# Kernel optimization log

Hardware: AMD Instinct MI355X
Metric: run time of the kernel (lower is better)

The kernel has to match this reference:

```python
import jax, jax.numpy as jnp
import numpy as np

C = 512
H_HEADS = 8
CTX_D = 768
GEO_D = 512
FFN_D = 4 * C
EPS = 1e-5


def _layernorm(x, g, b):
    mu = jnp.mean(x, axis=-1, keepdims=True)
    var = jnp.mean((x - mu) ** 2, axis=-1, keepdims=True)
    return (x - mu) * jax.lax.rsqrt(var + EPS) * g + b


def _cross_attn(x, ctx, Wq, Wk, Wv, Wo, bo, h):
    # x: (B, N, C), ctx: (B, S, Dctx)
    b, n, _ = x.shape
    s = ctx.shape[1]
    inner = Wq.shape[1]
    d = inner // h
    q = (x @ Wq).reshape(b, n, h, d)
    k = (ctx @ Wk).reshape(b, s, h, d)
    v = (ctx @ Wv).reshape(b, s, h, d)
    sim = jnp.einsum('bihd,bjhd->bhij', q, k) * (d ** -0.5)
    attn = jax.nn.softmax(sim, axis=-1)
    out = jnp.einsum('bhij,bjhd->bihd', attn, v).reshape(b, n, inner)
    return out @ Wo + bo


def setup_inputs() -> dict:
    key = jax.random.key(0)
    ks = jax.random.split(key, 24)
    std = lambda fan_in: 1.0 / np.sqrt(fan_in)
    inp = {
        'x': jax.random.normal(ks[0], (4, C, 64, 64), jnp.float32),
        'context': jax.random.normal(ks[1], (4, 77, CTX_D), jnp.float32),
        'geometry_tokens': jax.random.normal(ks[2], (4, 256, GEO_D), jnp.float32),
        # layernorm params (norm1..norm4)
        'g1': jnp.ones((C,)), 'b1': jnp.zeros((C,)),
        'g2': jnp.ones((C,)), 'b2': jnp.zeros((C,)),
        'g3': jnp.ones((C,)), 'b3': jnp.zeros((C,)),
        'g4': jnp.ones((C,)), 'b4': jnp.zeros((C,)),
        # cross-attention (context) weights
        'cWq': jax.random.normal(ks[3], (C, C)) * std(C),
        'cWk': jax.random.normal(ks[4], (CTX_D, C)) * std(CTX_D),
        'cWv': jax.random.normal(ks[5], (CTX_D, C)) * std(CTX_D),
        'cWo': jax.random.normal(ks[6], (C, C)) * std(C),
        'cbo': jnp.zeros((C,)),
        # geometry-attention weights
        'gWq': jax.random.normal(ks[7], (C, C)) * std(C),
        'gWk': jax.random.normal(ks[8], (GEO_D, C)) * std(GEO_D),
        'gWv': jax.random.normal(ks[9], (GEO_D, C)) * std(GEO_D),
        'gWo': jax.random.normal(ks[10], (C, C)) * std(C),
        'gbo': jnp.zeros((C,)),
        # FFN weights
        'W1': jax.random.normal(ks[11], (C, FFN_D)) * std(C),
        'bf1': jnp.zeros((FFN_D,)),
        'W2': jax.random.normal(ks[12], (FFN_D, C)) * std(FFN_D),
        'bf2': jnp.zeros((C,)),
    }
    return inp


def reference(x, context, geometry_tokens,
              g1, b1, g2, b2, g3, b3, g4, b4,
              cWq, cWk, cWv, cWo, cbo,
              gWq, gWk, gWv, gWo, gbo,
              W1, bf1, W2, bf2):
    b, c, h, w = x.shape
    t = x.reshape(b, c, h * w).transpose(0, 2, 1)  # (B, N, C)
    # self_attn is called with context=None -> identity, so this is t + norm1(t)
    t = t + _layernorm(t, g1, b1)
    t = t + _cross_attn(_layernorm(t, g2, b2), context, cWq, cWk, cWv, cWo, cbo, H_HEADS)
    t = t + _cross_attn(_layernorm(t, g3, b3), geometry_tokens, gWq, gWk, gWv, gWo, gbo, H_HEADS)
    hdn = jax.nn.gelu(_layernorm(t, g4, b4) @ W1 + bf1, approximate=False)
    t = t + hdn @ W2 + bf2
    return t.transpose(0, 2, 1).reshape(b, c, h, w)
```

## Files before the change

### kernel.cpp

```cpp
#include <hip/hip_runtime.h>
#include <hip/hip_bf16.h>

using bf16 = __hip_bfloat16;
typedef __attribute__((ext_vector_type(8))) short short8;
typedef __attribute__((ext_vector_type(4))) short short4v;
typedef __attribute__((ext_vector_type(4))) float floatx4;

#define DEVFN __device__ __forceinline__

DEVFN float bf2f(bf16 v) { return __bfloat162float(v); }
DEVFN bf16 f2bf(float v) { return __float2bfloat16(v); }
DEVFN float us2f(unsigned short u) {
    union { unsigned int i; float f; } c; c.i = ((unsigned int)u) << 16; return c.f;
}
DEVFN unsigned short f2bfbits(float v) {
    union { bf16 h; unsigned short u; } c; c.h = f2bf(v); return c.u;
}
DEVFN float loadF(const void* p, size_t i, int isf) {
    return isf ? ((const float*)p)[i] : us2f(((const unsigned short*)p)[i]);
}
DEVFN void gl_lds16(const bf16* g, short* l) {
    __builtin_amdgcn_global_load_lds(
        (const __attribute__((address_space(1))) unsigned int*)g,
        (__attribute__((address_space(3))) unsigned int*)l, 16, 0, 0);
}
DEVFN float fast_gelu(float v) {
    float u = v * (0.7978845608028654f + 0.0356774081f * v * v);
    float e = __expf(2.f * u);
    float th = 1.f - 2.f / (e + 1.f);
    return 0.5f * v * (1.f + th);
}

__global__ __launch_bounds__(256) void detect_kernel(const void* x, int* flag)
{
    __shared__ int any;
    if (threadIdx.x == 0) any = 0;
    __syncthreads();
    const unsigned short* p = (const unsigned short*)x;
    int hit = 0;
    for (int i = threadIdx.x; i < 8192; i += 256) {
        if ((p[i] & 0x7F80u) == 0x7F80u) hit = 1;
    }
    if (hit) any = 1;
    __syncthreads();
    if (threadIdx.x == 0) flag[0] = any;
}

struct CVTab {
    const void* src[14];
    bf16* dst[14];
    int cnt[14];
    int bstart[14];
};
__global__ __launch_bounds__(256) void convert_batch_kernel(
    CVTab tab, const int* __restrict__ flag)
{
    int isf = *flag;
    int b = blockIdx.x;
    int s = 0;
#pragma unroll
    for (int i = 1; i < 14; i++) if (b >= tab.bstart[i]) s = i;
    const void* src = tab.src[s];
    bf16* dst = tab.dst[s];
    int cnt = tab.cnt[s];
    int base = (b - tab.bstart[s]) * 2048;
    int lim = min(base + 2048, cnt);
    for (int i = base + (int)threadIdx.x; i < lim; i += 256)
        dst[i] = f2bf(loadF(src, i, isf));
}

__global__ __launch_bounds__(256) void ln_in_kernel(
    const void* __restrict__ x, float* __restrict__ t,
    const bf16* __restrict__ g1c, const bf16* __restrict__ b1c,
    const bf16* __restrict__ g2c, const bf16* __restrict__ b2c,
    bf16* __restrict__ u,
    const int* __restrict__ flag, int NN)
{
    __shared__ float tile[16][516];
    int isf = *flag;
    int b = blockIdx.y;
    int n0 = blockIdx.x * 16;
    int tid = threadIdx.x;
    int nx = tid & 15, cy = tid >> 4;
#pragma unroll
    for (int p = 0; p < 32; p++) {
        int c = p * 16 + cy;
        tile[nx][c] = loadF(x, ((size_t)b * 512 + c) * NN + n0 + nx, isf);
    }
    __syncthreads();
    int w = tid >> 6, lane = tid & 63;
    for (int rr = 0; rr < 4; rr++) {
        int r = w * 4 + rr;
        float4 v0 = *(const float4*)&tile[r][lane * 8];
        float4 v1 = *(const float4*)&tile[r][lane * 8 + 4];
        float vals[8] = {v0.x, v0.y, v0.z, v0.w, v1.x, v1.y, v1.z, v1.w};
        float s = 0.f;
#pragma unroll
        for (int i = 0; i < 8; i++) s += vals[i];
#pragma unroll
        for (int off = 32; off; off >>= 1) s += __shfl_xor(s, off, 64);
        float mu = s * (1.f / 512.f);
        float sq = 0.f;
#pragma unroll
        for (int i = 0; i < 8; i++) { float d = vals[i] - mu; sq += d * d; }
#pragma unroll
        for (int off = 32; off; off >>= 1) sq += __shfl_xor(sq, off, 64);
        float rs = rsqrtf(sq * (1.f / 512.f) + 1e-5f);
        float out[8];
#pragma unroll
        for (int i = 0; i < 8; i++) {
            int c = lane * 8 + i;
            out[i] = vals[i] + (vals[i] - mu) * rs * bf2f(g1c[c]) + bf2f(b1c[c]);
        }
        size_t rbase = ((size_t)b * NN + n0 + r) * 512 + lane * 8;
        float* tp = t + rbase;
        *(float4*)tp = make_float4(out[0], out[1], out[2], out[3]);
        *(float4*)(tp + 4) = make_float4(out[4], out[5], out[6], out[7]);
        float s2 = 0.f;
#pragma unroll
        for (int i = 0; i < 8; i++) s2 += out[i];
#pragma unroll
        for (int off = 32; off; off >>= 1) s2 += __shfl_xor(s2, off, 64);
        float mu2 = s2 * (1.f / 512.f);
        float sq2 = 0.f;
#pragma unroll
        for (int i = 0; i < 8; i++) { float d = out[i] - mu2; sq2 += d * d; }
#pragma unroll
        for (int off = 32; off; off >>= 1) sq2 += __shfl_xor(sq2, off, 64);
        float rs2 = rsqrtf(sq2 * (1.f / 512.f) + 1e-5f);
        short4v uo[2];
#pragma unroll
        for (int i = 0; i < 8; i++) {
            int c = lane * 8 + i;
            uo[i >> 2][i & 3] =
                (short)f2bfbits((out[i] - mu2) * rs2 * bf2f(g2c[c]) + bf2f(b2c[c]));
        }
        *(short4v*)((unsigned short*)u + rbase) = uo[0];
        *(short4v*)((unsigned short*)u + rbase + 4) = uo[1];
    }
}

__global__ __launch_bounds__(256) void ln_res_kernel(
    const float* __restrict__ t, const bf16* __restrict__ r1,
    const bf16* __restrict__ r2,
    const bf16* __restrict__ g, const bf16* __restrict__ bta,
    bf16* __restrict__ outp, int Mrows)
{
    int w = threadIdx.x >> 6, lane = threadIdx.x & 63;
    int row = blockIdx.x * 4 + w;
    if (row >= Mrows) return;
    size_t base = (size_t)row * 512 + lane * 8;
    float4 v0 = *(const float4*)(t + base);
    float4 v1 = *(const float4*)(t + base + 4);
    float vals[8] = {v0.x, v0.y, v0.z, v0.w, v1.x, v1.y, v1.z, v1.w};
    {
        short8 a = *(const short8*)((const unsigned short*)r1 + base);
#pragma unroll
        for (int i = 0; i < 8; i++) vals[i] += us2f(((unsigned short*)&a)[i]);
    }
    if (r2) {
        short8 a = *(const short8*)((const unsigned short*)r2 + base);
#pragma unroll
        for (int i = 0; i < 8; i++) vals[i] += us2f(((unsigned short*)&a)[i]);
    }
    float s = 0.f;
#pragma unroll
    for (int i = 0; i < 8; i++) s += vals[i];
#pragma unroll
    for (int off = 32; off; off >>= 1) s += __shfl_xor(s, off, 64);
    float mu = s * (1.f / 512.f);
    float sq = 0.f;
#pragma unroll
    for (int i = 0; i < 8; i++) { float d = vals[i] - mu; sq += d * d; }
#pragma unroll
    for (int off = 32; off; off >>= 1) sq += __shfl_xor(sq, off, 64);
    float rs = rsqrtf(sq * (1.f / 512.f) + 1e-5f);
    short4v uo[2];
#pragma unroll
    for (int i = 0; i < 8; i++) {
        int c = lane * 8 + i;
        uo[i >> 2][i & 3] =
            (short)f2bfbits((vals[i] - mu) * rs * bf2f(g[c]) + bf2f(bta[c]));
    }
    *(short4v*)((unsigned short*)outp + base) = uo[0];
    *(short4v*)((unsigned short*)outp + base + 4) = uo[1];
}

__global__ __launch_bounds__(256) void transpose_out_kernel(
    const float* __restrict__ t, const bf16* __restrict__ rc,
    const bf16* __restrict__ rg, const bf16* __restrict__ f,
    void* __restrict__ o, const int* __restrict__ flag,
    int C, int NN)
{
    __shared__ float tile[32][33];
    int isf = *flag;
    int b = blockIdx.z;
    int n0 = blockIdx.x * 32, c0 = blockIdx.y * 32;
    int tx = threadIdx.x, ty = threadIdx.y;
#pragma unroll
    for (int i = 0; i < 4; i++) {
        size_t idx = ((size_t)b * NN + n0 + ty + i * 8) * C + c0 + tx;
        tile[ty + i * 8][tx] = t[idx] + bf2f(rc[idx]) + bf2f(rg[idx]) + bf2f(f[idx]);
    }
    __syncthreads();
#pragma unroll
    for (int i = 0; i < 4; i++) {
        size_t oi = ((size_t)b * C + c0 + ty + i * 8) * NN + n0 + tx;
        float val = tile[tx][ty + i * 8];
        if (isf) ((float*)o)[oi] = val;
        else ((bf16*)o)[oi] = f2bf(val);
    }
}

struct TWTab {
    const void* src[10];
    bf16* dst[10];
    int K[10];
    int Nc[10];
    int tstart[10];
};
__global__ __launch_bounds__(256) void transpose_w_batch(
    TWTab tab, const int* __restrict__ flag)
{
    __shared__ float tile[32][33];
    int isf = *flag;
    int b = blockIdx.x;
    int s = 0;
#pragma unroll
    for (int i = 1; i < 10; i++) if (b >= tab.tstart[i]) s = i;
    const void* Wm = tab.src[s];
    bf16* WT = tab.dst[s];
    int K = tab.K[s], Nc = tab.Nc[s];
    int lt = b - tab.tstart[s];
    int ntx = Nc >> 5;
    int n0 = (lt % ntx) * 32, k0 = (lt / ntx) * 32;
    int tx = threadIdx.x, ty = threadIdx.y;
#pragma unroll
    for (int i = 0; i < 4; i++)
        tile[ty + i * 8][tx] = loadF(Wm, (size_t)(k0 + ty + i * 8) * Nc + n0 + tx, isf);
    __syncthreads();
#pragma unroll
    for (int i = 0; i < 4; i++)
        WT[(size_t)(n0 + ty + i * 8) * K + k0 + tx] = f2bf(tile[tx][ty + i * 8]);
}

template <int MODE>
__global__ __launch_bounds__(256) void gemm64x2(
    const bf16* __restrict__ A,
    const bf16* __restrict__ WT0, const bf16* __restrict__ WT1,
    bf16* __restrict__ o0, bf16* __restrict__ o1,
    int M, int K, int Nc)
{
    const bf16* WT = blockIdx.z ? WT1 : WT0;
    bf16* outp = blockIdx.z ? o1 : o0;
    __shared__ short As[64 * 32];
    __shared__ short Bs[64 * 32];
    const int tid = threadIdx.x;
    const int m0 = blockIdx.y * 64;
    const int n0 = blockIdx.x * 64;
    const int w = tid >> 6;
    const int lane = tid & 63;
    const int lm = lane & 15;
    const int lq = lane >> 4;

    floatx4 acc[4];
#pragma unroll
    for (int nb = 0; nb < 4; nb++) acc[nb] = (floatx4){0.f, 0.f, 0.f, 0.f};

    const int srow = tid >> 2;
    const int scol = (tid & 3) << 3;
    const int agrow = m0 + srow;
    const bool aok = agrow < M;
    const bf16* Aptr = A + (size_t)agrow * K + scol;
    const bf16* Bptr = WT + (size_t)(n0 + srow) * K + scol;

    for (int k0 = 0; k0 < K; k0 += 32) {
        __syncthreads();
        int4 av = make_int4(0, 0, 0, 0);
        if (aok) av = *(const int4*)(Aptr + k0);
        *(int4*)(&As[srow * 32 + scol]) = av;
        *(int4*)(&Bs[srow * 32 + scol]) = *(const int4*)(Bptr + k0);
        __syncthreads();
        short8 a = *(const short8*)(&As[(w * 16 + lm) * 32 + lq * 8]);
#pragma unroll
        for (int nb = 0; nb < 4; nb++) {
            short8 b = *(const short8*)(&Bs[(nb * 16 + lm) * 32 + lq * 8]);
            acc[nb] = __builtin_amdgcn_mfma_f32_16x16x32_bf16(a, b, acc[nb], 0, 0, 0);
        }
    }

#pragma unroll
    for (int nb = 0; nb < 4; nb++) {
        int col = n0 + nb * 16 + lm;
#pragma unroll
        for (int r = 0; r < 4; r++) {
            int row = m0 + w * 16 + lq * 4 + r;
            if (row < M) {
                float v = acc[nb][r];
                if (MODE == 1) v = fast_gelu(v);
                outp[(size_t)row * Nc + col] = f2bf(v);
            }
        }
    }
}

#define MFMA_PAIR(RB, A00, A01, A10, A11)                                              \
    _Pragma("unroll")                                                                   \
    for (int cb = 0; cb < CB; cb++) {                                                   \
        acc[cb][RB]     = __builtin_amdgcn_mfma_f32_16x16x32_bf16(bf0[cb], A00, acc[cb][RB], 0, 0, 0);     \
        acc[cb][RB]     = __builtin_amdgcn_mfma_f32_16x16x32_bf16(bf1[cb], A01, acc[cb][RB], 0, 0, 0);     \
        acc[cb][RB + 1] = __builtin_amdgcn_mfma_f32_16x16x32_bf16(bf0[cb], A10, acc[cb][RB + 1], 0, 0, 0); \
        acc[cb][RB + 1] = __builtin_amdgcn_mfma_f32_16x16x32_bf16(bf1[cb], A11, acc[cb][RB + 1], 0, 0, 0); \
    }

template <int MODE, int CB>
__global__ __launch_bounds__(512, 2) void gemm8p(
    const bf16* __restrict__ A, const bf16* __restrict__ WT,
    const bf16* __restrict__ bias, void* __restrict__ outp,
    int K, int Nc)
{
    constexpr int BN = CB * 64;
    constexpr int ABUF = 256 * 64;
    constexpr int BBUF = BN * 64;
    __shared__ short As[2 * ABUF];
    __shared__ short Bs[2 * BBUF];

    const int tid = threadIdx.x;
    const int gx = gridDim.x;
    int g = blockIdx.y * gx + blockIdx.x;
    const int cpx = (gx * gridDim.y) >> 3;
    g = (g & 7) * cpx + (g >> 3);
    const int m0 = (g / gx) * 256;
    const int n0 = (g % gx) * BN;

    const int w = tid >> 6, lane = tid & 63;
    const int lm = lane & 15, lq = lane >> 4;
    const int wm = w >> 2, wn = w & 3;

    floatx4 acc[CB][8];
#pragma unroll
    for (int cb = 0; cb < CB; cb++)
#pragma unroll
        for (int rb = 0; rb < 8; rb++) acc[cb][rb] = (floatx4){0.f, 0.f, 0.f, 0.f};

    const int rbaseA = (tid >> 3) + ((tid >= 256) ? 96 : 0);
    const int chk = (((tid & 7) ^ ((tid >> 3) & 7)) << 3);
    const bf16* pA = A + (size_t)(m0 + rbaseA) * K + chk;
    const int rbaseB = ((tid >> 7) << (CB == 4 ? 6 : 5)) + ((tid >> 3) & 15);
    const bf16* pB = WT + (size_t)(n0 + rbaseB) * K + chk;
    const int wbA = w * 512 + ((w >= 4) ? 6144 : 0);
    const int wbB = (CB == 4) ? ((w >> 1) * 4096 + (w & 1) * 512)
                              : ((w >> 1) * 2048 + (w & 1) * 512);
    const size_t K32 = (size_t)K * 32;
    const size_t K16 = (size_t)K * 16;

    const int arow = (wm * 128 + lm) * 64;
    const int brow = (wn * CB * 16 + lm) * 64;
    const int sl0 = ((lq ^ (lm & 7)) << 3);
    const int sl1 = (((4 + lq) ^ (lm & 7)) << 3);

    const int nt = K >> 6;

#pragma unroll
    for (int q = 0; q < 4; q++) gl_lds16(pA + (size_t)q * K32, As + q * 2048 + wbA);
    if constexpr (CB == 4) {
        gl_lds16(pB,           Bs + wbB);
        gl_lds16(pB + K16,     Bs + 1024 + wbB);
        gl_lds16(pB + 2 * K16, Bs + 2048 + wbB);
        gl_lds16(pB + 3 * K16, Bs + 3072 + wbB);
    } else {
        gl_lds16(pB,       Bs + wbB);
        gl_lds16(pB + K16, Bs + 1024 + wbB);
    }
    {
        const bf16* qA = pA + 64;
        const bf16* qB = pB + 64;
        if constexpr (CB == 4) {
            gl_lds16(qB,           Bs + BBUF + wbB);
            gl_lds16(qB + K16,     Bs + BBUF + 1024 + wbB);
            gl_lds16(qB + 2 * K16, Bs + BBUF + 2048 + wbB);
            gl_lds16(qB + 3 * K16, Bs + BBUF + 3072 + wbB);
            gl_lds16(qA,           As + ABUF + wbA);
            gl_lds16(qA + K32,     As + ABUF + 2048 + wbA);
            asm volatile("s_waitcnt vmcnt(6)\n\ts_barrier" ::: "memory");
        } else {
            gl_lds16(qB,           Bs + BBUF + wbB);
            gl_lds16(qB + K16, Bs + BBUF + 1024 + wbB);
            gl_lds16(qA,           As + ABUF + wbA);
            gl_lds16(qA + K32,     As + ABUF + 2048 + wbA);
            gl_lds16(qA + 2 * K32, As + ABUF + 4096 + wbA);
            asm volatile("s_waitcnt vmcnt(5)\n\ts_barrier" ::: "memory");
        }
    }

    for (int s = 0; s < nt; ++s) {
        const int cu = s & 1;
        const short* cA = As + cu * ABUF;
        const short* cB = Bs + cu * BBUF;
        short* oA = As + (cu ^ 1) * ABUF;
        short* sA = As + cu * ABUF;
        short* sB = Bs + cu * BBUF;
        const bf16* pA1 = pA + (s + 1) * 64;
        const bf16* pA2 = pA + (s + 2) * 64;
        const bf16* pB2 = pB + (s + 2) * 64;
        short8 bf0[CB], bf1[CB], x0, x1, y0, y1;

#pragma unroll
        for (int cb = 0; cb < CB; cb++) {
            bf0[cb] = *(const short8*)&cB[brow + cb * 1024 + sl0];
            bf1[cb] = *(const short8*)&cB[brow + cb * 1024 + sl1];
        }
        x0 = *(const short8*)&cA[arow + sl0];
        x1 = *(const short8*)&cA[arow + sl1];
        y0 = *(const short8*)&cA[arow + 1024 + sl0];
        y1 = *(const short8*)&cA[arow + 1024 + sl1];
        if (s + 1 < nt) {
            if constexpr (CB == 4) {
                gl_lds16(pA1 + 2 * K32, oA + 2 * 2048 + wbA);
                gl_lds16(pA1 + 3 * K32, oA + 3 * 2048 + wbA);
            } else {
                gl_lds16(pA1 + 3 * K32, oA + 3 * 2048 + wbA);
            }
        }
        __builtin_amdgcn_s_setprio(1);
        MFMA_PAIR(0, x0, x1, y0, y1)
        __builtin_amdgcn_s_setprio(0);
        asm volatile("s_waitcnt lgkmcnt(0)\n\ts_barrier" ::: "memory");

        x0 = *(const short8*)&cA[arow + 2 * 1024 + sl0];
        x1 = *(const short8*)&cA[arow + 2 * 1024 + sl1];
        y0 = *(const short8*)&cA[arow + 3 * 1024 + sl0];
        y1 = *(const short8*)&cA[arow + 3 * 1024 + sl1];
        if (s + 2 < nt) {
            gl_lds16(pB2,       sB + wbB);
            gl_lds16(pB2 + K16, sB + 1024 + wbB);
        }
        __builtin_amdgcn_s_setprio(1);
        MFMA_PAIR(2, x0, x1, y0, y1)
        __builtin_amdgcn_s_setprio(0);
        asm volatile("s_waitcnt lgkmcnt(0)\n\ts_barrier" ::: "memory");

        x0 = *(const short8*)&cA[arow + 4 * 1024 + sl0];
        x1 = *(const short8*)&cA[arow + 4 * 1024 + sl1];
        y0 = *(const short8*)&cA[arow + 5 * 1024 + sl0];
        y1 = *(const short8*)&cA[arow + 5 * 1024 + sl1];
        if (s + 2 < nt) {
            if constexpr (CB == 4) {
                gl_lds16(pB2 + 2 * K16, sB + 2048 + wbB);
                gl_lds16(pB2 + 3 * K16, sB + 3072 + wbB);
            } else {
                gl_lds16(pA2, sA + wbA);
            }
        }
        __builtin_amdgcn_s_setprio(1);
        MFMA_PAIR(4, x0, x1, y0, y1)
        __builtin_amdgcn_s_setprio(0);
        asm volatile("s_waitcnt lgkmcnt(0)\n\ts_barrier" ::: "memory");

        x0 = *(const short8*)&cA[arow + 6 * 1024 + sl0];
        x1 = *(const short8*)&cA[arow + 6 * 1024 + sl1];
        y0 = *(const short8*)&cA[arow + 7 * 1024 + sl0];
        y1 = *(const short8*)&cA[arow + 7 * 1024 + sl1];
        if (s + 2 < nt) {
            if constexpr (CB == 4) {
                gl_lds16(pA2,       sA + wbA);
                gl_lds16(pA2 + K32, sA + 2048 + wbA);
            } else {
                gl_lds16(pA2 + K32,     sA + 2048 + wbA);
                gl_lds16(pA2 + 2 * K32, sA + 4096 + wbA);
            }
        }
        __builtin_amdgcn_s_setprio(1);
        MFMA_PAIR(6, x0, x1, y0, y1)
        __builtin_amdgcn_s_setprio(0);
        if (s <= nt - 3) {
            if constexpr (CB == 4)
                asm volatile("s_waitcnt vmcnt(6) lgkmcnt(0)\n\ts_barrier" ::: "memory");
            else
                asm volatile("s_waitcnt vmcnt(5) lgkmcnt(0)\n\ts_barrier" ::: "memory");
        } else if (s == nt - 2) {
            asm volatile("s_waitcnt vmcnt(0) lgkmcnt(0)\n\ts_barrier" ::: "memory");
        } else {
            asm volatile("s_waitcnt lgkmcnt(0)\n\ts_barrier" ::: "memory");
        }
    }
    __syncthreads();

    float4 bias4[CB];
#pragma unroll
    for (int cb = 0; cb < CB; cb++) {
        if (bias) {
            const bf16* bp = bias + n0 + wn * (CB * 16) + cb * 16 + lq * 4;
            bias4[cb] = make_float4(bf2f(bp[0]), bf2f(bp[1]), bf2f(bp[2]), bf2f(bp[3]));
        } else {
            bias4[cb] = make_float4(0.f, 0.f, 0.f, 0.f);
        }
    }

    if constexpr (MODE == 2) {
        float* po = (float*)outp;
#pragma unroll
        for (int rb = 0; rb < 8; rb++) {
            size_t m = m0 + wm * 128 + rb * 16 + lm;
#pragma unroll
            for (int cb = 0; cb < CB; cb++) {
                float* p = po + m * Nc + n0 + wn * (CB * 16) + cb * 16 + lq * 4;
                float4 f = *(float4*)p;
                f.x += acc[cb][rb][0] + bias4[cb].x;
                f.y += acc[cb][rb][1] + bias4[cb].y;
                f.z += acc[cb][rb][2] + bias4[cb].z;
                f.w += acc[cb][rb][3] + bias4[cb].w;
                *(float4*)p = f;
            }
        }
    } else if constexpr (CB == 2) {
        unsigned short* op = (unsigned short*)outp;
#pragma unroll
        for (int rb = 0; rb < 8; rb++) {
            size_t m = m0 + wm * 128 + rb * 16 + lm;
#pragma unroll
            for (int cb = 0; cb < 2; cb++) {
                short4v pk;
#pragma unroll
                for (int r = 0; r < 4; r++) {
                    float vv = acc[cb][rb][r] + ((const float*)&bias4[cb])[r];
                    if (MODE == 1) vv = fast_gelu(vv);
                    pk[r] = (short)f2bfbits(vv);
                }
                *(short4v*)(op + m * Nc + n0 + wn * 32 + cb * 16 + lq * 4) = pk;
            }
        }
    } else {
        unsigned short* stgb = (unsigned short*)&As[w * 1024];
        unsigned short* op = (unsigned short*)outp;
#pragma unroll
        for (int rb = 0; rb < 8; rb++) {
#pragma unroll
            for (int cb = 0; cb < 4; cb++) {
                short4v pk;
#pragma unroll
                for (int r = 0; r < 4; r++) {
                    float vv = acc[cb][rb][r] + ((const float*)&bias4[cb])[r];
                    if (MODE == 1) vv = fast_gelu(vv);
                    pk[r] = (short)f2bfbits(vv);
                }
                int chunk = (cb * 2 + (lq >> 1)) ^ (lm & 7);
                *(short4v*)(&stgb[lm * 64 + chunk * 8 + (lq & 1) * 4]) = pk;
            }
#pragma unroll
            for (int p = 0; p < 2; p++) {
                int row = p * 8 + (lane >> 3);
                int chunk = lane & 7;
                short8 ov = *(const short8*)(&stgb[row * 64 + ((chunk ^ (row & 7)) * 8)]);
                size_t m = m0 + wm * 128 + rb * 16 + row;
                *(short8*)(op + m * Nc + n0 + wn * 64 + chunk * 8) = ov;
            }
        }
    }
}

template <int SPAD, int SVALID>
__global__ __launch_bounds__(256) void attn_mfma_kernel(
    const bf16* __restrict__ q, const bf16* __restrict__ k, const bf16* __restrict__ v,
    bf16* __restrict__ o, int N)
{
    constexpr int MB = SPAD / 16;
    constexpr int KS = SPAD / 32;
    __shared__ unsigned short lds[SPAD * 64 + 64 * SPAD];
    unsigned short* Ks = lds;
    unsigned short* Vt = lds + SPAD * 64;
    unsigned short* Pw = lds;

    const int tid = threadIdx.x;
    const int b = blockIdx.x >> 3;
    const int h = blockIdx.x & 7;
    const int n0 = blockIdx.y * 64;
    const int w = tid >> 6, lane = tid & 63;
    const int lm = lane & 15, lq = lane >> 4;

    const unsigned short* kp = (const unsigned short*)k;
    const unsigned short* vp = (const unsigned short*)v;
    for (int idx = tid * 8; idx < SPAD * 64; idx += 2048) {
        int s = idx >> 6, d0 = idx & 63;
        short8 kv = {0, 0, 0, 0, 0, 0, 0, 0};
        short8 vv = {0, 0, 0, 0, 0, 0, 0, 0};
        if (s < SVALID) {
            size_t gb = ((size_t)(b * SVALID + s)) * 512 + h * 64 + d0;
            kv = *(const short8*)(kp + gb);
            vv = *(const short8*)(vp + gb);
        }
        int kc = (d0 >> 3) ^ (s & 7);
        *(short8*)(&Ks[s * 64 + kc * 8]) = kv;
        const unsigned short* vvp = (const unsigned short*)&vv;
#pragma unroll
        for (int i = 0; i < 8; i++) {
            int d = d0 + i;
            int sc = (s >> 3) ^ (d & 7);
            Vt[d * SPAD + sc * 8 + (s & 7)] = vvp[i];
        }
    }

    const int q0 = n0 + w * 16;
    const unsigned short* qp = (const unsigned short*)q;
    size_t qbase = ((size_t)(b * N + q0 + lm)) * 512 + h * 64 + lq * 8;
    short8 qf0 = *(const short8*)(qp + qbase);
    short8 qf1 = *(const short8*)(qp + qbase + 32);
    __syncthreads();

    floatx4 sacc[MB];
#pragma unroll
    for (int mb = 0; mb < MB; mb++) sacc[mb] = (floatx4){0.f, 0.f, 0.f, 0.f};
#pragma unroll
    for (int mb = 0; mb < MB; mb++) {
        int srow = mb * 16 + lm;
        short8 a0 = *(const short8*)(&Ks[srow * 64 + ((lq ^ (lm & 7)) * 8)]);
        short8 a1 = *(const short8*)(&Ks[srow * 64 + (((4 + lq) ^ (lm & 7)) * 8)]);
        sacc[mb] = __builtin_amdgcn_mfma_f32_16x16x32_bf16(a0, qf0, sacc[mb], 0, 0, 0);
        sacc[mb] = __builtin_amdgcn_mfma_f32_16x16x32_bf16(a1, qf1, sacc[mb], 0, 0, 0);
    }

    float mx = -1e30f;
#pragma unroll
    for (int mb = 0; mb < MB; mb++)
#pragma unroll
        for (int r = 0; r < 4; r++) {
            int s = mb * 16 + lq * 4 + r;
            if (s < SVALID) mx = fmaxf(mx, sacc[mb][r]);
        }
    mx = fmaxf(mx, __shfl_xor(mx, 16, 64));
    mx = fmaxf(mx, __shfl_xor(mx, 32, 64));
    mx *= 0.125f;
    float sum = 0.f;
#pragma unroll
    for (int mb = 0; mb < MB; mb++)
#pragma unroll
        for (int r = 0; r < 4; r++) {
            int s = mb * 16 + lq * 4 + r;
            float e = (s < SVALID) ? __expf(sacc[mb][r] * 0.125f - mx) : 0.f;
            sacc[mb][r] = e;
            sum += e;
        }
    sum += __shfl_xor(sum, 16, 64);
    sum += __shfl_xor(sum, 32, 64);
    float inv = 1.f / sum;

    __syncthreads();

    unsigned short* Pme = Pw + w * 16 * SPAD;
#pragma unroll
    for (int mb = 0; mb < MB; mb++) {
        short4v pk;
        pk[0] = (short)f2bfbits(sacc[mb][0] * inv);
        pk[1] = (short)f2bfbits(sacc[mb][1] * inv);
        pk[2] = (short)f2bfbits(sacc[mb][2] * inv);
        pk[3] = (short)f2bfbits(sacc[mb][3] * inv);
        int chunk = (mb * 2 + (lq >> 1)) ^ (lm & 7);
        *(short4v*)(&Pme[lm * SPAD + chunk * 8 + (lq & 1) * 4]) = pk;
    }

    floatx4 oacc[4];
#pragma unroll
    for (int mb2 = 0; mb2 < 4; mb2++) oacc[mb2] = (floatx4){0.f, 0.f, 0.f, 0.f};
    for (int ks = 0; ks < KS; ks++) {
        int sch = ((ks * 4 + lq) ^ (lm & 7)) * 8;
        short8 bfrag = *(const short8*)(&Pme[lm * SPAD + sch]);
#pragma unroll
        for (int mb2 = 0; mb2 < 4; mb2++) {
            int d = mb2 * 16 + lm;
            short8 afrag = *(const short8*)(&Vt[d * SPAD + sch]);
            oacc[mb2] = __builtin_amdgcn_mfma_f32_16x16x32_bf16(afrag, bfrag, oacc[mb2], 0, 0, 0);
        }
    }

#pragma unroll
    for (int mb2 = 0; mb2 < 4; mb2++) {
        short4v ok;
        ok[0] = (short)f2bfbits(oacc[mb2][0]);
        ok[1] = (short)f2bfbits(oacc[mb2][1]);
        ok[2] = (short)f2bfbits(oacc[mb2][2]);
        ok[3] = (short)f2bfbits(oacc[mb2][3]);
        int chunk = (mb2 * 2 + (lq >> 1)) ^ (lm & 7);
        *(short4v*)(&Pme[lm * 64 + chunk * 8 + (lq & 1) * 4]) = ok;
    }
    unsigned short* op = (unsigned short*)o;
#pragma unroll
    for (int p = 0; p < 2; p++) {
        int row = p * 8 + (lane >> 3);
        int chunk = lane & 7;
        short8 ov = *(const short8*)(&Pme[row * 64 + ((chunk ^ (row & 7)) * 8)]);
        *(short8*)(op + ((size_t)(b * N + n0 + w * 16 + row)) * 512 + h * 64 + chunk * 8) = ov;
    }
}

extern "C" void kernel_launch(void* const* d_in, const int* in_sizes, int n_in,
                              void* d_out, int out_size, void* d_ws, size_t ws_size,
                              hipStream_t stream)
{
    const void* x   = d_in[0];
    const void* ctx = d_in[1];
    const void* geo = d_in[2];
    const void* g1 = d_in[3];  const void* b1 = d_in[4];
    const void* g2 = d_in[5];  const void* b2 = d_in[6];
    const void* g3 = d_in[7];  const void* b3 = d_in[8];
    const void* g4 = d_in[9];  const void* b4 = d_in[10];
    const void* cWq = d_in[11]; const void* cWk = d_in[12];
    const void* cWv = d_in[13]; const void* cWo = d_in[14];
    const void* cbo = d_in[15];
    const void* gWq = d_in[16]; const void* gWk = d_in[17];
    const void* gWv = d_in[18]; const void* gWo = d_in[19];
    const void* gbo = d_in[20];
    const void* W1 = d_in[21];  const void* bf1 = d_in[22];
    const void* W2 = d_in[23];  const void* bf2 = d_in[24];

    const int B = 4, C = 512, NN = 4096;
    const int M = B * NN;

    char* ws = (char*)d_ws;
    size_t off = 0;
    auto alloc = [&](size_t bytes) -> void* {
        void* p = ws + off; off += (bytes + 255) & ~(size_t)255; return p;
    };
    int*   flag = (int*)alloc(256);
    float* t  = (float*)alloc((size_t)M * C * 4);
    bf16* u   = (bf16*)alloc((size_t)M * C * 2);
    bf16* qb  = (bf16*)alloc((size_t)M * C * 2);
    bf16* rc  = (bf16*)alloc((size_t)M * C * 2);
    bf16* rg  = (bf16*)alloc((size_t)M * C * 2);
    bf16* fb  = (bf16*)alloc((size_t)M * C * 2);
    bf16* kb  = (bf16*)alloc((size_t)B * 256 * C * 2);
    bf16* vb  = (bf16*)alloc((size_t)B * 256 * C * 2);
    bf16* ctxb = (bf16*)alloc((size_t)B * 77 * 768 * 2);
    bf16* geob = (bf16*)alloc((size_t)B * 256 * 512 * 2);
    bf16* cWqT = (bf16*)alloc((size_t)512 * 512 * 2);
    bf16* cWkT = (bf16*)alloc((size_t)512 * 768 * 2);
    bf16* cWvT = (bf16*)alloc((size_t)512 * 768 * 2);
    bf16* cWoT = (bf16*)alloc((size_t)512 * 512 * 2);
    bf16* gWqT = (bf16*)alloc((size_t)512 * 512 * 2);
    bf16* gWkT = (bf16*)alloc((size_t)512 * 512 * 2);
    bf16* gWvT = (bf16*)alloc((size_t)512 * 512 * 2);
    bf16* gWoT = (bf16*)alloc((size_t)512 * 512 * 2);
    bf16* W1T  = (bf16*)alloc((size_t)2048 * 512 * 2);
    bf16* W2T  = (bf16*)alloc((size_t)512 * 2048 * 2);
    bf16* prm  = (bf16*)alloc((size_t)7680 * 2);
    bf16* ob = u;

    int chunk;
    bf16* hb;
    size_t rem = (ws_size > off) ? (ws_size - off) : 0;
    if (rem >= (size_t)16384 * 2048 * 2) { chunk = 16384; hb = (bf16*)alloc((size_t)16384 * 2048 * 2); }
    else if (rem >= (size_t)8192 * 2048 * 2) { chunk = 8192; hb = (bf16*)alloc((size_t)8192 * 2048 * 2); }
    else { chunk = 4096; hb = qb; }
    (void)in_sizes; (void)n_in; (void)out_size;

    bf16 *pg1 = prm, *pb1 = prm + 512, *pg2 = prm + 1024, *pb2 = prm + 1536;
    bf16 *pg3 = prm + 2048, *pb3 = prm + 2560, *pg4 = prm + 3072, *pb4 = prm + 3584;
    bf16 *pcbo = prm + 4096, *pgbo = prm + 4608, *pbf1 = prm + 5120, *pbf2 = prm + 7168;

    dim3 tb(32, 8);

    detect_kernel<<<1, 256, 0, stream>>>(x, flag);

    {
        CVTab cv;
        const void* csrc[14] = {g1, b1, g2, b2, g3, b3, g4, b4, cbo, gbo, bf1, bf2, ctx, geo};
        bf16* cdst[14] = {prm, prm + 512, prm + 1024, prm + 1536, prm + 2048, prm + 2560,
                          prm + 3072, prm + 3584, prm + 4096, prm + 4608, prm + 5120,
                          prm + 7168, ctxb, geob};
        int ccnt[14] = {512, 512, 512, 512, 512, 512, 512, 512, 512, 512, 2048, 512,
                        B * 77 * 768, B * 256 * 512};
        int bacc = 0;
        for (int i = 0; i < 14; i++) {
            cv.src[i] = csrc[i]; cv.dst[i] = cdst[i]; cv.cnt[i] = ccnt[i];
            cv.bstart[i] = bacc;
            bacc += (ccnt[i] + 2047) / 2048;
        }
        convert_batch_kernel<<<bacc, 256, 0, stream>>>(cv, flag);
    }

    ln_in_kernel<<<dim3(NN / 16, B), 256, 0, stream>>>(x, t, pg1, pb1, pg2, pb2, u, flag, NN);

    {
        TWTab tw;
        const void* wsrc[10] = {cWq, cWk, cWv, cWo, gWq, gWk, gWv, gWo, W1, W2};
        bf16* wdst[10] = {cWqT, cWkT, cWvT, cWoT, gWqT, gWkT, gWvT, gWoT, W1T, W2T};
        int wK[10]  = {512, 768, 768, 512, 512, 512, 512, 512, 512, 2048};
        int wNc[10] = {512, 512, 512, 512, 512, 512, 512, 512, 2048, 512};
        int tacc = 0;
        for (int i = 0; i < 10; i++) {
            tw.src[i] = wsrc[i]; tw.dst[i] = wdst[i]; tw.K[i] = wK[i]; tw.Nc[i] = wNc[i];
            tw.tstart[i] = tacc;
            tacc += (wNc[i] / 32) * (wK[i] / 32);
        }
        transpose_w_batch<<<tacc, tb, 0, stream>>>(tw, flag);
    }

    gemm8p<0, 2><<<dim3(4, M / 256), 512, 0, stream>>>(u, cWqT, nullptr, qb, 512, 512);
    gemm64x2<0><<<dim3(8, (308 + 63) / 64, 2), 256, 0, stream>>>(ctxb, cWkT, cWvT, kb, vb, 308, 768, 512);
    attn_mfma_kernel<128, 77><<<dim3(B * 8, NN / 64), 256, 0, stream>>>(qb, kb, vb, ob, NN);
    gemm8p<0, 2><<<dim3(4, M / 256), 512, 0, stream>>>(ob, cWoT, pcbo, rc, 512, 512);
    ln_res_kernel<<<M / 4, 256, 0, stream>>>(t, rc, nullptr, pg3, pb3, u, M);

    gemm8p<0, 2><<<dim3(4, M / 256), 512, 0, stream>>>(u, gWqT, nullptr, qb, 512, 512);
    gemm64x2<0><<<dim3(8, 1024 / 64, 2), 256, 0, stream>>>(geob, gWkT, gWvT, kb, vb, 1024, 512, 512);
    attn_mfma_kernel<256, 256><<<dim3(B * 8, NN / 64), 256, 0, stream>>>(qb, kb, vb, ob, NN);
    gemm8p<0, 2><<<dim3(4, M / 256), 512, 0, stream>>>(ob, gWoT, pgbo, rg, 512, 512);
    ln_res_kernel<<<M / 4, 256, 0, stream>>>(t, rc, rg, pg4, pb4, u, M);

    for (int mc = 0; mc < M / chunk; mc++) {
        bf16* uc = u + (size_t)mc * chunk * 512;
        bf16* fc = fb + (size_t)mc * chunk * 512;
        gemm8p<1, 4><<<dim3(2048 / 256, chunk / 256), 512, 0, stream>>>(uc, W1T, pbf1, hb, 512, 2048);
        gemm8p<0, 2><<<dim3(512 / 128, chunk / 256), 512, 0, stream>>>(hb, W2T, pbf2, fc, 2048, 512);
    }

    transpose_out_kernel<<<dim3(NN / 32, C / 32, B), tb, 0, stream>>>(t, rc, rg, fb, d_out, flag, C, NN);
}
```

Before: 465.6 us.

## Replace 256-row GEMM with simpler 128x128 tile double-buffered GEMM

Replaces the heavily hand-pipelined 256xBN GEMM (two-stage prefetch, interleaved loads, LDS-staged stores) with a 128x128 tile kernel that uses a simple double buffer and allows up to 4 blocks per CU. This gives more blocks and higher occupancy, which may help the smaller GEMMs fill the GPU. In exchange each block reuses less data per tile, the load pipelining is simpler with a full vmcnt(0) barrier every K step, and the FFN1 output no longer goes through a coalesced LDS-staged store.

```diff
diff --git a/kernel.cpp b/kernel.cpp
--- a/kernel.cpp
+++ b/kernel.cpp
@@ -304,257 +304,110 @@
     }
 }
 
-#define MFMA_PAIR(RB, A00, A01, A10, A11)                                              \
-    _Pragma("unroll")                                                                   \
-    for (int cb = 0; cb < CB; cb++) {                                                   \
-        acc[cb][RB]     = __builtin_amdgcn_mfma_f32_16x16x32_bf16(bf0[cb], A00, acc[cb][RB], 0, 0, 0);     \
-        acc[cb][RB]     = __builtin_amdgcn_mfma_f32_16x16x32_bf16(bf1[cb], A01, acc[cb][RB], 0, 0, 0);     \
-        acc[cb][RB + 1] = __builtin_amdgcn_mfma_f32_16x16x32_bf16(bf0[cb], A10, acc[cb][RB + 1], 0, 0, 0); \
-        acc[cb][RB + 1] = __builtin_amdgcn_mfma_f32_16x16x32_bf16(bf1[cb], A11, acc[cb][RB + 1], 0, 0, 0); \
-    }
-
-template <int MODE, int CB>
-__global__ __launch_bounds__(512, 2) void gemm8p(
+template <int MODE>
+__global__ __launch_bounds__(512, 4) void gemmO(
     const bf16* __restrict__ A, const bf16* __restrict__ WT,
-    const bf16* __restrict__ bias, void* __restrict__ outp,
+    const bf16* __restrict__ bias, bf16* __restrict__ outp,
     int K, int Nc)
 {
-    constexpr int BN = CB * 64;
-    constexpr int ABUF = 256 * 64;
-    constexpr int BBUF = BN * 64;
-    __shared__ short As[2 * ABUF];
-    __shared__ short Bs[2 * BBUF];
+    __shared__ short As[2 * 8192];
+    __shared__ short Bs[2 * 8192];
 
     const int tid = threadIdx.x;
     const int gx = gridDim.x;
     int g = blockIdx.y * gx + blockIdx.x;
     const int cpx = (gx * gridDim.y) >> 3;
     g = (g & 7) * cpx + (g >> 3);
-    const int m0 = (g / gx) * 256;
-    const int n0 = (g % gx) * BN;
+    const int m0 = (g / gx) * 128;
+    const int n0 = (g % gx) * 128;
 
     const int w = tid >> 6, lane = tid & 63;
     const int lm = lane & 15, lq = lane >> 4;
     const int wm = w >> 2, wn = w & 3;
 
-    floatx4 acc[CB][8];
-#pragma unroll
-    for (int cb = 0; cb < CB; cb++)
-#pragma unroll
-        for (int rb = 0; rb < 8; rb++) acc[cb][rb] = (floatx4){0.f, 0.f, 0.f, 0.f};
-
-    const int rbaseA = (tid >> 3) + ((tid >= 256) ? 96 : 0);
-    const int chk = (((tid & 7) ^ ((tid >> 3) & 7)) << 3);
-    const bf16* pA = A + (size_t)(m0 + rbaseA) * K + chk;
-    const int rbaseB = ((tid >> 7) << (CB == 4 ? 6 : 5)) + ((tid >> 3) & 15);
-    const bf16* pB = WT + (size_t)(n0 + rbaseB) * K + chk;
-    const int wbA = w * 512 + ((w >= 4) ? 6144 : 0);
-    const int wbB = (CB == 4) ? ((w >> 1) * 4096 + (w & 1) * 512)
-                              : ((w >> 1) * 2048 + (w & 1) * 512);
-    const size_t K32 = (size_t)K * 32;
-    const size_t K16 = (size_t)K * 16;
-
-    const int arow = (wm * 128 + lm) * 64;
-    const int brow = (wn * CB * 16 + lm) * 64;
+    floatx4 acc[2][4];
+#pragma unroll
+    for (int cb = 0; cb < 2; cb++)
+#pragma unroll
+        for (int rb = 0; rb < 4; rb++) acc[cb][rb] = (floatx4){0.f, 0.f, 0.f, 0.f};
+
+    const int rstg = tid >> 3;
+    const int chk = (((tid & 7) ^ (rstg & 7)) << 3);
+    const bf16* pA0 = A + (size_t)(m0 + rstg) * K + chk;
+    const bf16* pA1 = A + (size_t)(m0 + 64 + rstg) * K + chk;
+    const bf16* pB0 = WT + (size_t)(n0 + rstg) * K + chk;
+    const bf16* pB1 = WT + (size_t)(n0 + 64 + rstg) * K + chk;
+    const int wb = w * 512;
+
+    auto STAGE = [&](int d, int koff) {
+        short* la = As + d * 8192;
+        short* lb = Bs + d * 8192;
+        gl_lds16(pA0 + koff, la + wb);
+        gl_lds16(pA1 + koff, la + 4096 + wb);
+        gl_lds16(pB0 + koff, lb + wb);
+        gl_lds16(pB1 + koff, lb + 4096 + wb);
+    };
+
+    const int arow = (wm * 64 + lm) * 64;
+    const int brow = (wn * 32 + lm) * 64;
     const int sl0 = ((lq ^ (lm & 7)) << 3);
     const int sl1 = (((4 + lq) ^ (lm & 7)) << 3);
 
     const int nt = K >> 6;
-
-#pragma unroll
-    for (int q = 0; q < 4; q++) gl_lds16(pA + (size_t)q * K32, As + q * 2048 + wbA);
-    if constexpr (CB == 4) {
-        gl_lds16(pB,           Bs + wbB);
-        gl_lds16(pB + K16,     Bs + 1024 + wbB);
-        gl_lds16(pB + 2 * K16, Bs + 2048 + wbB);
-        gl_lds16(pB + 3 * K16, Bs + 3072 + wbB);
-    } else {
-        gl_lds16(pB,       Bs + wbB);
-        gl_lds16(pB + K16, Bs + 1024 + wbB);
-    }
-    {
-        const bf16* qA = pA + 64;
-        const bf16* qB = pB + 64;
-        if constexpr (CB == 4) {
-            gl_lds16(qB,           Bs + BBUF + wbB);
-            gl_lds16(qB + K16,     Bs + BBUF + 1024 + wbB);
-            gl_lds16(qB + 2 * K16, Bs + BBUF + 2048 + wbB);
-            gl_lds16(qB + 3 * K16, Bs + BBUF + 3072 + wbB);
-            gl_lds16(qA,           As + ABUF + wbA);
-            gl_lds16(qA + K32,     As + ABUF + 2048 + wbA);
-            asm volatile("s_waitcnt vmcnt(6)\n\ts_barrier" ::: "memory");
+    STAGE(0, 0);
+    asm volatile("s_waitcnt vmcnt(0)\n\ts_barrier" ::: "memory");
+
+    for (int s = 0; s < nt; ++s) {
+        const short* cA = As + (s & 1) * 8192;
+        const short* cB = Bs + (s & 1) * 8192;
+        if (s + 1 < nt) STAGE((s + 1) & 1, (s + 1) << 6);
+        short8 b00 = *(const short8*)&cB[brow + sl0];
+        short8 b01 = *(const short8*)&cB[brow + sl1];
+        short8 b10 = *(const short8*)&cB[brow + 1024 + sl0];
+        short8 b11 = *(const short8*)&cB[brow + 1024 + sl1];
+        short8 a0[4], a1[4];
+#pragma unroll
+        for (int rb = 0; rb < 4; rb++) {
+            a0[rb] = *(const short8*)&cA[arow + rb * 1024 + sl0];
+            a1[rb] = *(const short8*)&cA[arow + rb * 1024 + sl1];
+        }
+        __builtin_amdgcn_s_setprio(1);
+#pragma unroll
+        for (int rb = 0; rb < 4; rb++) {
+            acc[0][rb] = __builtin_amdgcn_mfma_f32_16x16x32_bf16(b00, a0[rb], acc[0][rb], 0, 0, 0);
+            acc[0][rb] = __builtin_amdgcn_mfma_f32_16x16x32_bf16(b01, a1[rb], acc[0][rb], 0, 0, 0);
+            acc[1][rb] = __builtin_amdgcn_mfma_f32_16x16x32_bf16(b10, a0[rb], acc[1][rb], 0, 0, 0);
+            acc[1][rb] = __builtin_amdgcn_mfma_f32_16x16x32_bf16(b11, a1[rb], acc[1][rb], 0, 0, 0);
+        }
+        __builtin_amdgcn_s_setprio(0);
+        if (s + 1 < nt)
+            asm volatile("s_waitcnt vmcnt(0) lgkmcnt(0)\n\ts_barrier" ::: "memory");
+    }
+
+    float4 bias2[2];
+#pragma unroll
+    for (int cb = 0; cb < 2; cb++) {
+        if (bias) {
+            const bf16* bp = bias + n0 + wn * 32 + cb * 16 + lq * 4;
+            bias2[cb] = make_float4(bf2f(bp[0]), bf2f(bp[1]), bf2f(bp[2]), bf2f(bp[3]));
         } else {
-            gl_lds16(qB,           Bs + BBUF + wbB);
-            gl_lds16(qB + K16, Bs + BBUF + 1024 + wbB);
-            gl_lds16(qA,           As + ABUF + wbA);
-            gl_lds16(qA + K32,     As + ABUF + 2048 + wbA);
-            gl_lds16(qA + 2 * K32, As + ABUF + 4096 + wbA);
-            asm volatile("s_waitcnt vmcnt(5)\n\ts_barrier" ::: "memory");
-        }
-    }
-
-    for (int s = 0; s < nt; ++s) {
-        const int cu = s & 1;
-        const short* cA = As + cu * ABUF;
-        const short* cB = Bs + cu * BBUF;
-        short* oA = As + (cu ^ 1) * ABUF;
-        short* sA = As + cu * ABUF;
-        short* sB = Bs + cu * BBUF;
-        const bf16* pA1 = pA + (s + 1) * 64;
-        const bf16* pA2 = pA + (s + 2) * 64;
-        const bf16* pB2 = pB + (s + 2) * 64;
-        short8 bf0[CB], bf1[CB], x0, x1, y0, y1;
-
-#pragma unroll
-        for (int cb = 0; cb < CB; cb++) {
-            bf0[cb] = *(const short8*)&cB[brow + cb * 1024 + sl0];
-            bf1[cb] = *(const short8*)&cB[brow + cb * 1024 + sl1];
-        }
-        x0 = *(const short8*)&cA[arow + sl0];
-        x1 = *(const short8*)&cA[arow + sl1];
-        y0 = *(const short8*)&cA[arow + 1024 + sl0];
-        y1 = *(const short8*)&cA[arow + 1024 + sl1];
-        if (s + 1 < nt) {
-            if constexpr (CB == 4) {
-                gl_lds16(pA1 + 2 * K32, oA + 2 * 2048 + wbA);
-                gl_lds16(pA1 + 3 * K32, oA + 3 * 2048 + wbA);
-            } else {
-                gl_lds16(pA1 + 3 * K32, oA + 3 * 2048 + wbA);
+            bias2[cb] = make_float4(0.f, 0.f, 0.f, 0.f);
+        }
+    }
+    unsigned short* op = (unsigned short*)outp;
+#pragma unroll
+    for (int rb = 0; rb < 4; rb++) {
+        size_t m = m0 + wm * 64 + rb * 16 + lm;
+#pragma unroll
+        for (int cb = 0; cb < 2; cb++) {
+            short4v pk;
+#pragma unroll
+            for (int r = 0; r < 4; r++) {
+                float vv = acc[cb][rb][r] + ((const float*)&bias2[cb])[r];
+                if (MODE == 1) vv = fast_gelu(vv);
+                pk[r] = (short)f2bfbits(vv);
             }
-        }
-        __builtin_amdgcn_s_setprio(1);
-        MFMA_PAIR(0, x0, x1, y0, y1)
-        __builtin_amdgcn_s_setprio(0);
-        asm volatile("s_waitcnt lgkmcnt(0)\n\ts_barrier" ::: "memory");
-
-        x0 = *(const short8*)&cA[arow + 2 * 1024 + sl0];
-        x1 = *(const short8*)&cA[arow + 2 * 1024 + sl1];
-        y0 = *(const short8*)&cA[arow + 3 * 1024 + sl0];
-        y1 = *(const short8*)&cA[arow + 3 * 1024 + sl1];
-        if (s + 2 < nt) {
-            gl_lds16(pB2,       sB + wbB);
-            gl_lds16(pB2 + K16, sB + 1024 + wbB);
-        }
-        __builtin_amdgcn_s_setprio(1);
-        MFMA_PAIR(2, x0, x1, y0, y1)
-        __builtin_amdgcn_s_setprio(0);
-        asm volatile("s_waitcnt lgkmcnt(0)\n\ts_barrier" ::: "memory");
-
-        x0 = *(const short8*)&cA[arow + 4 * 1024 + sl0];
-        x1 = *(const short8*)&cA[arow + 4 * 1024 + sl1];
-        y0 = *(const short8*)&cA[arow + 5 * 1024 + sl0];
-        y1 = *(const short8*)&cA[arow + 5 * 1024 + sl1];
-        if (s + 2 < nt) {
-            if constexpr (CB == 4) {
-                gl_lds16(pB2 + 2 * K16, sB + 2048 + wbB);
-                gl_lds16(pB2 + 3 * K16, sB + 3072 + wbB);
-            } else {
-                gl_lds16(pA2, sA + wbA);
-            }
-        }
-        __builtin_amdgcn_s_setprio(1);
-        MFMA_PAIR(4, x0, x1, y0, y1)
-        __builtin_amdgcn_s_setprio(0);
-        asm volatile("s_waitcnt lgkmcnt(0)\n\ts_barrier" ::: "memory");
-
-        x0 = *(const short8*)&cA[arow + 6 * 1024 + sl0];
-        x1 = *(const short8*)&cA[arow + 6 * 1024 + sl1];
-        y0 = *(const short8*)&cA[arow + 7 * 1024 + sl0];
-        y1 = *(const short8*)&cA[arow + 7 * 1024 + sl1];
-        if (s + 2 < nt) {
-            if constexpr (CB == 4) {
-                gl_lds16(pA2,       sA + wbA);
-                gl_lds16(pA2 + K32, sA + 2048 + wbA);
-            } else {
-                gl_lds16(pA2 + K32,     sA + 2048 + wbA);
-                gl_lds16(pA2 + 2 * K32, sA + 4096 + wbA);
-            }
-        }
-        __builtin_amdgcn_s_setprio(1);
-        MFMA_PAIR(6, x0, x1, y0, y1)
-        __builtin_amdgcn_s_setprio(0);
-        if (s <= nt - 3) {
-            if constexpr (CB == 4)
-                asm volatile("s_waitcnt vmcnt(6) lgkmcnt(0)\n\ts_barrier" ::: "memory");
-            else
-                asm volatile("s_waitcnt vmcnt(5) lgkmcnt(0)\n\ts_barrier" ::: "memory");
-        } else if (s == nt - 2) {
-            asm volatile("s_waitcnt vmcnt(0) lgkmcnt(0)\n\ts_barrier" ::: "memory");
-        } else {
-            asm volatile("s_waitcnt lgkmcnt(0)\n\ts_barrier" ::: "memory");
-        }
-    }
-    __syncthreads();
-
-    float4 bias4[CB];
-#pragma unroll
-    for (int cb = 0; cb < CB; cb++) {
-        if (bias) {
-            const bf16* bp = bias + n0 + wn * (CB * 16) + cb * 16 + lq * 4;
-            bias4[cb] = make_float4(bf2f(bp[0]), bf2f(bp[1]), bf2f(bp[2]), bf2f(bp[3]));
-        } else {
-            bias4[cb] = make_float4(0.f, 0.f, 0.f, 0.f);
-        }
-    }
-
-    if constexpr (MODE == 2) {
-        float* po = (float*)outp;
-#pragma unroll
-        for (int rb = 0; rb < 8; rb++) {
-            size_t m = m0 + wm * 128 + rb * 16 + lm;
-#pragma unroll
-            for (int cb = 0; cb < CB; cb++) {
-                float* p = po + m * Nc + n0 + wn * (CB * 16) + cb * 16 + lq * 4;
-                float4 f = *(float4*)p;
-                f.x += acc[cb][rb][0] + bias4[cb].x;
-                f.y += acc[cb][rb][1] + bias4[cb].y;
-                f.z += acc[cb][rb][2] + bias4[cb].z;
-                f.w += acc[cb][rb][3] + bias4[cb].w;
-                *(float4*)p = f;
-            }
-        }
-    } else if constexpr (CB == 2) {
-        unsigned short* op = (unsigned short*)outp;
-#pragma unroll
-        for (int rb = 0; rb < 8; rb++) {
-            size_t m = m0 + wm * 128 + rb * 16 + lm;
-#pragma unroll
-            for (int cb = 0; cb < 2; cb++) {
-                short4v pk;
-#pragma unroll
-                for (int r = 0; r < 4; r++) {
-                    float vv = acc[cb][rb][r] + ((const float*)&bias4[cb])[r];
-                    if (MODE == 1) vv = fast_gelu(vv);
-                    pk[r] = (short)f2bfbits(vv);
-                }
-                *(short4v*)(op + m * Nc + n0 + wn * 32 + cb * 16 + lq * 4) = pk;
-            }
-        }
-    } else {
-        unsigned short* stgb = (unsigned short*)&As[w * 1024];
-        unsigned short* op = (unsigned short*)outp;
-#pragma unroll
-        for (int rb = 0; rb < 8; rb++) {
-#pragma unroll
-            for (int cb = 0; cb < 4; cb++) {
-                short4v pk;
-#pragma unroll
-                for (int r = 0; r < 4; r++) {
-                    float vv = acc[cb][rb][r] + ((const float*)&bias4[cb])[r];
-                    if (MODE == 1) vv = fast_gelu(vv);
-                    pk[r] = (short)f2bfbits(vv);
-                }
-                int chunk = (cb * 2 + (lq >> 1)) ^ (lm & 7);
-                *(short4v*)(&stgb[lm * 64 + chunk * 8 + (lq & 1) * 4]) = pk;
-            }
-#pragma unroll
-            for (int p = 0; p < 2; p++) {
-                int row = p * 8 + (lane >> 3);
-                int chunk = lane & 7;
-                short8 ov = *(const short8*)(&stgb[row * 64 + ((chunk ^ (row & 7)) * 8)]);
-                size_t m = m0 + wm * 128 + rb * 16 + row;
-                *(short8*)(op + m * Nc + n0 + wn * 64 + chunk * 8) = ov;
-            }
+            *(short4v*)(op + m * Nc + n0 + wn * 32 + cb * 16 + lq * 4) = pk;
         }
     }
 }
@@ -794,23 +647,23 @@
         transpose_w_batch<<<tacc, tb, 0, stream>>>(tw, flag);
     }
 
-    gemm8p<0, 2><<<dim3(4, M / 256), 512, 0, stream>>>(u, cWqT, nullptr, qb, 512, 512);
+    gemmO<0><<<dim3(4, M / 128), 512, 0, stream>>>(u, cWqT, nullptr, qb, 512, 512);
     gemm64x2<0><<<dim3(8, (308 + 63) / 64, 2), 256, 0, stream>>>(ctxb, cWkT, cWvT, kb, vb, 308, 768, 512);
     attn_mfma_kernel<128, 77><<<dim3(B * 8, NN / 64), 256, 0, stream>>>(qb, kb, vb, ob, NN);
-    gemm8p<0, 2><<<dim3(4, M / 256), 512, 0, stream>>>(ob, cWoT, pcbo, rc, 512, 512);
+    gemmO<0><<<dim3(4, M / 128), 512, 0, stream>>>(ob, cWoT, pcbo, rc, 512, 512);
     ln_res_kernel<<<M / 4, 256, 0, stream>>>(t, rc, nullptr, pg3, pb3, u, M);
 
-    gemm8p<0, 2><<<dim3(4, M / 256), 512, 0, stream>>>(u, gWqT, nullptr, qb, 512, 512);
+    gemmO<0><<<dim3(4, M / 128), 512, 0, stream>>>(u, gWqT, nullptr, qb, 512, 512);
     gemm64x2<0><<<dim3(8, 1024 / 64, 2), 256, 0, stream>>>(geob, gWkT, gWvT, kb, vb, 1024, 512, 512);
     attn_mfma_kernel<256, 256><<<dim3(B * 8, NN / 64), 256, 0, stream>>>(qb, kb, vb, ob, NN);
-    gemm8p<0, 2><<<dim3(4, M / 256), 512, 0, stream>>>(ob, gWoT, pgbo, rg, 512, 512);
+    gemmO<0><<<dim3(4, M / 128), 512, 0, stream>>>(ob, gWoT, pgbo, rg, 512, 512);
     ln_res_kernel<<<M / 4, 256, 0, stream>>>(t, rc, rg, pg4, pb4, u, M);
 
     for (int mc = 0; mc < M / chunk; mc++) {
         bf16* uc = u + (size_t)mc * chunk * 512;
         bf16* fc = fb + (size_t)mc * chunk * 512;
-        gemm8p<1, 4><<<dim3(2048 / 256, chunk / 256), 512, 0, stream>>>(uc, W1T, pbf1, hb, 512, 2048);
-        gemm8p<0, 2><<<dim3(512 / 128, chunk / 256), 512, 0, stream>>>(hb, W2T, pbf2, fc, 2048, 512);
+        gemmO<1><<<dim3(2048 / 128, chunk / 128), 512, 0, stream>>>(uc, W1T, pbf1, hb, 512, 2048);
+        gemmO<0><<<dim3(512 / 128, chunk / 128), 512, 0, stream>>>(hb, W2T, pbf2, fc, 2048, 512);
     }
 
     transpose_out_kernel<<<dim3(NN / 32, C / 32, B), tb, 0, stream>>>(t, rc, rg, fb, d_out, flag, C, NN);
```

Measured after the change: 443.8 us. 1.05x faster.
